# Performance work log

Measured on AMD Instinct MI355X. Metric: run time of the kernel, lower is better.

## Reference

```python
import jax, jax.numpy as jnp
import numpy as np

N, E = 50000, 600000
IN_DIM, HID, OUT_DIM = 128, 256, 64


def _sage_conv(x, edge_index, W_l, W_r, b):
    # PyG SAGEConv (mean aggr, root_weight=True):
    # out = mean_{j in N(i)} x_j @ W_l + x_i @ W_r + b
    src, dst = edge_index[0], edge_index[1]
    msg = x[src]  # [E, d] gather
    agg = jax.ops.segment_sum(msg, dst, num_segments=N)  # [N, d]
    cnt = jax.ops.segment_sum(jnp.ones((E,), dtype=x.dtype), dst, num_segments=N)
    agg = agg / jnp.maximum(cnt, 1.0)[:, None]
    return agg @ W_l + x @ W_r + b


def setup_inputs() -> dict:
    key = jax.random.key(0)
    ks = jax.random.split(key, 8)
    x = jax.random.normal(ks[0], (N, IN_DIM), dtype=jnp.float32)
    edge_index = jax.random.randint(ks[1], (2, E), 0, N, dtype=jnp.int64)
    s1 = 1.0 / np.sqrt(IN_DIM)
    s2 = 1.0 / np.sqrt(HID)
    W1_l = jax.random.uniform(ks[2], (IN_DIM, HID), jnp.float32, -s1, s1)
    W1_r = jax.random.uniform(ks[3], (IN_DIM, HID), jnp.float32, -s1, s1)
    b1 = jnp.zeros((HID,), jnp.float32)
    W2_l = jax.random.uniform(ks[4], (HID, OUT_DIM), jnp.float32, -s2, s2)
    W2_r = jax.random.uniform(ks[5], (HID, OUT_DIM), jnp.float32, -s2, s2)
    b2 = jnp.zeros((OUT_DIM,), jnp.float32)
    return {"x": x, "edge_index": edge_index, "W1_l": W1_l, "W1_r": W1_r,
            "b1": b1, "W2_l": W2_l, "W2_r": W2_r, "b2": b2}


def reference(x, edge_index, W1_l, W1_r, b1, W2_l, W2_r, b2):
    # SAGE.forward, eval mode (dropout = identity)
    h = jax.nn.relu(_sage_conv(x, edge_index, W1_l, W1_r, b1))
    out = _sage_conv(h, edge_index, W2_l, W2_r, b2)
    return out
```

## Files before the change

### kernel.cpp

```cpp
#include <hip/hip_runtime.h>

#define N_NODES 50000
#define N_EDGES 600000
#define N_PAD   50048
#define IN_DIM 128
#define HID 256
#define OUT_DIM 64
#define MAX_DEG 64
#define NBINS 196
#define BCAP 4096
#define NPART 256
#define ECHUNK 2344

typedef __attribute__((ext_vector_type(4))) float f32x4;
typedef __attribute__((ext_vector_type(8))) short short8;
typedef unsigned short u16;
typedef unsigned int u32;

__device__ __forceinline__ float bf2f(u32 lo16) {
  u32 u = lo16 << 16;
  return __builtin_bit_cast(float, u);
}
__device__ __forceinline__ u16 f2bf(float f) {
  u32 u = __builtin_bit_cast(u32, f);
  u = (u + 0x7FFF + ((u >> 16) & 1)) >> 16;
  return (u16)u;
}

#define SEG0 (N_PAD * 16)
#define SEG1 (SEG0 + 128 * 64)
#define SEG2 (SEG1 + 64 * 64)
#define PREP_TOT SEG2

__global__ void k_prep_part(const float* __restrict__ x,
                            const float* __restrict__ W1l, const float* __restrict__ W1r,
                            const float* __restrict__ W2l, const float* __restrict__ W2r,
                            const int* __restrict__ src, const int* __restrict__ dst,
                            u16* __restrict__ xb, u16* __restrict__ W1p,
                            u16* __restrict__ W2p, u32* __restrict__ region,
                            int* __restrict__ gcur) {
  if (blockIdx.x < NPART) {
    __shared__ int hist[256];
    __shared__ int base[256];
    const int t = threadIdx.x;
    hist[t] = 0;
    __syncthreads();
    const int e0 = blockIdx.x * ECHUNK;
    const int e1 = min(e0 + ECHUNK, N_EDGES);
    for (int e = e0 + t; e < e1; e += 256) atomicAdd(&hist[dst[e] >> 8], 1);
    __syncthreads();
    base[t] = (hist[t] > 0) ? atomicAdd(&gcur[t], hist[t]) : 0;
    hist[t] = 0;
    __syncthreads();
    for (int e = e0 + t; e < e1; e += 256) {
      int d = dst[e];
      int bin = d >> 8;
      int idx = base[bin] + atomicAdd(&hist[bin], 1);
      if (idx < BCAP)
        region[(size_t)bin * BCAP + idx] = (u32)(src[e] & 0xffff) | ((u32)(d & 255) << 16);
    }
    return;
  }
  int idx = (blockIdx.x - NPART) * 256 + threadIdx.x;
  if (idx < SEG0) {
    int row = idx >> 4;
    int c8 = (idx & 15) * 8;
    short8 o;
    if (row < N_NODES) {
      f32x4 a = *(const f32x4*)&x[(size_t)row * 128 + c8];
      f32x4 b = *(const f32x4*)&x[(size_t)row * 128 + c8 + 4];
      o[0] = (short)f2bf(a[0]); o[1] = (short)f2bf(a[1]);
      o[2] = (short)f2bf(a[2]); o[3] = (short)f2bf(a[3]);
      o[4] = (short)f2bf(b[0]); o[5] = (short)f2bf(b[1]);
      o[6] = (short)f2bf(b[2]); o[7] = (short)f2bf(b[3]);
    } else {
      for (int j = 0; j < 8; ++j) o[j] = 0;
    }
    *(short8*)&xb[(size_t)row * 128 + c8] = o;
  } else if (idx < SEG1) {
    int i = idx - SEG0;
    int F = i >> 6, l = i & 63;
    int wch = F >> 6, kt = (F >> 4) & 3, kk = (F >> 3) & 1, n = F & 7;
    int row = wch * 128 + n * 16 + (l & 15);
    int kb = kt * 64 + kk * 32 + (l >> 4) * 8;
    short8 o;
#pragma unroll
    for (int j = 0; j < 8; ++j) {
      int k = kb + j;
      float v = (k < 128) ? W1l[(size_t)k * HID + row] : W1r[(size_t)(k - 128) * HID + row];
      o[j] = (short)f2bf(v);
    }
    *(short8*)&W1p[(size_t)i * 8] = o;
  } else if (idx < SEG2) {
    int i = idx - SEG1;
    int G = i >> 6, l = i & 63;
    int wch = G >> 5, kk = (G >> 2) & 7, n = G & 3;
    int row = wch * 64 + n * 16 + (l & 15);
    int kb = kk * 32 + (l >> 4) * 8;
    short8 o;
#pragma unroll
    for (int j = 0; j < 8; ++j) {
      int k = kb + j;
      float v = (row < 64) ? W2l[(size_t)k * OUT_DIM + row]
                           : W2r[(size_t)k * OUT_DIM + (row - 64)];
      o[j] = (short)f2bf(v);
    }
    *(short8*)&W2p[(size_t)i * 8] = o;
  }
}


__global__ __launch_bounds__(256) void k_build(const u32* __restrict__ region,
                                               const int* __restrict__ gcur,
                                               int* __restrict__ cnt,
                                               u16* __restrict__ bucket) {
  __shared__ u16 lbkt[256 * 64];
  __shared__ int lcnt[256];
  const int t = threadIdx.x;
  const int bin = blockIdx.x;
  lcnt[t] = 0;
  __syncthreads();
  int n = gcur[bin];
  if (n > BCAP) n = BCAP;
  for (int i = t; i < n; i += 256) {
    u32 r = region[(size_t)bin * BCAP + i];
    int dl = (r >> 16) & 255;
    int pos = atomicAdd(&lcnt[dl], 1);
    if (pos < MAX_DEG) lbkt[dl * 64 + pos] = (u16)(r & 0xffff);
  }
  __syncthreads();
  int gnode = bin * 256 + t;
  if (gnode < N_NODES) cnt[gnode] = lcnt[t];
  for (int i = t; i < 2048; i += 256) {
    int nl = i >> 3, sub = i & 7;
    int gn = bin * 256 + nl;
    if (gn < N_NODES)
      *(short8*)&bucket[(size_t)gn * 64 + sub * 8] = *(const short8*)&lbkt[nl * 64 + sub * 8];
  }
}


__global__ void k_agg(const u16* __restrict__ xb, const int* __restrict__ cnt,
                      const u16* __restrict__ bucket, u16* __restrict__ agg) {
  int node = blockIdx.x * 4 + (threadIdx.x >> 6);
  if (node >= N_PAD) return;
  int lane = threadIdx.x & 63;
  int es = lane >> 4, dl = lane & 15;
  int deg = (node < N_NODES) ? cnt[node] : 0;
  int sreg = (node < N_NODES) ? (int)bucket[(size_t)node * MAX_DEG + lane] : 0;
  float acc[8] = {0.f, 0.f, 0.f, 0.f, 0.f, 0.f, 0.f, 0.f};
  short8 pend = (short8){0, 0, 0, 0, 0, 0, 0, 0};
  for (int e = 0; e < deg; e += 4) {
    int ee = e + es;
    int s = __shfl(sreg, ee & 63);
    short8 v = (short8){0, 0, 0, 0, 0, 0, 0, 0};
    if (ee < deg) v = *(const short8*)&xb[(size_t)s * 128 + dl * 8];
#pragma unroll
    for (int j = 0; j < 8; ++j) acc[j] += bf2f((u16)pend[j]);
    pend = v;
  }
#pragma unroll
  for (int j = 0; j < 8; ++j) acc[j] += bf2f((u16)pend[j]);
#pragma unroll
  for (int j = 0; j < 8; ++j) {
    acc[j] += __shfl_xor(acc[j], 16);
    acc[j] += __shfl_xor(acc[j], 32);
  }
  float inv = 1.f / fmaxf((float)deg, 1.f);
  if (es == 0) {
    short8 o;
#pragma unroll
    for (int j = 0; j < 8; ++j) o[j] = (short)f2bf(acc[j] * inv);
    *(short8*)&agg[(size_t)node * 128 + dl * 8] = o;
  }
}


__device__ __forceinline__ void gl_lds16(const void* g, void* l) {
  __builtin_amdgcn_global_load_lds((const __attribute__((address_space(1))) u32*)g,
                                   (__attribute__((address_space(3))) u32*)l, 16, 0, 0);
}

__global__ __launch_bounds__(256, 3) void k_mlp(
    const u16* __restrict__ agg, const u16* __restrict__ xb,
    const u16* __restrict__ W1p, const u16* __restrict__ W2p,
    const float* __restrict__ b1, u16* __restrict__ pb, u16* __restrict__ qb) {
  __shared__ u16 hs[64 * 256];
  __shared__ u16 As[2][64 * 64];
  const int t = threadIdx.x;
  const int wave = t >> 6;
  const int lane = t & 63;
  const int brow = blockIdx.x * 64;
  const int lr = lane & 15;
  const int kg = lane >> 4;
  const int wch = wave & 1;

  const int wr = (wave >> 1) * 32;
  const int wc = wch * 128;

  f32x4 acc[2][8];
#pragma unroll
  for (int m = 0; m < 2; ++m)
#pragma unroll
    for (int n = 0; n < 8; ++n) acc[m][n] = (f32x4){0.f, 0.f, 0.f, 0.f};

  auto stageA = [&](int buf, int kt) {
    const u16* base = (kt < 2) ? agg : xb;
    const int koff = (kt & 1) * 64;
#pragma unroll
    for (int i = 0; i < 2; ++i) {
      int chunk = wave * 2 + i;
      int f = chunk * 1024 + lane * 16;
      int row = f >> 7;
      int cbs = (f & 127) ^ ((row & 7) << 4);
      gl_lds16(&base[(size_t)(brow + row) * 128 + koff + (cbs >> 1)],
               (char*)As[buf] + chunk * 1024);
    }
  };

  stageA(0, 0);
  __syncthreads();

#pragma unroll
  for (int kt = 0; kt < 4; ++kt) {
    const int cur = kt & 1;
    if (kt < 3) stageA(cur ^ 1, kt + 1);
#pragma unroll
    for (int kk = 0; kk < 2; ++kk) {
      short8 af[2], bfr[8];
      const int cb = kk * 64 + kg * 16;
#pragma unroll
      for (int m = 0; m < 2; ++m) {
        int row = wr + m * 16 + lr;
        af[m] = *(const short8*)((const char*)As[cur] + row * 128 + (cb ^ ((row & 7) << 4)));
      }
#pragma unroll
      for (int n = 0; n < 8; ++n)
        bfr[n] = *(const short8*)&W1p[(size_t)(((wch * 4 + kt) * 2 + kk) * 8 + n) * 512 +
                                      lane * 8];
#pragma unroll
      for (int m = 0; m < 2; ++m)
#pragma unroll
        for (int n = 0; n < 8; ++n)
          acc[m][n] =
              __builtin_amdgcn_mfma_f32_16x16x32_bf16(af[m], bfr[n], acc[m][n], 0, 0, 0);
    }
    __syncthreads();
  }

#pragma unroll
  for (int n = 0; n < 8; ++n) {
    int col = wc + n * 16 + lr;
    float bv = b1[col];
#pragma unroll
    for (int m = 0; m < 2; ++m) {
#pragma unroll
      for (int j = 0; j < 4; ++j) {
        int row = wr + kg * 4 + m * 16 + j;
        float v = fmaxf(acc[m][n][j] + bv, 0.f);
        *(u16*)((char*)hs + row * 512 + ((col * 2) ^ ((row & 7) << 4))) = f2bf(v);
      }
    }
  }
  __syncthreads();

  const int wr2 = (wave >> 1) * 32;
  f32x4 acc2[2][4];
#pragma unroll
  for (int m = 0; m < 2; ++m)
#pragma unroll
    for (int n = 0; n < 4; ++n) acc2[m][n] = (f32x4){0.f, 0.f, 0.f, 0.f};

#pragma unroll
  for (int kk = 0; kk < 8; ++kk) {
    const int cb = kk * 64 + kg * 16;
    short8 af[2], bfr[4];
#pragma unroll
    for (int m = 0; m < 2; ++m) {
      int row = wr2 + m * 16 + lr;
      af[m] = *(const short8*)((const char*)hs + row * 512 + (cb ^ ((row & 7) << 4)));
    }
#pragma unroll
    for (int n = 0; n < 4; ++n)
      bfr[n] = *(const short8*)&W2p[(size_t)((wch * 8 + kk) * 4 + n) * 512 + lane * 8];
#pragma unroll
    for (int m = 0; m < 2; ++m)
#pragma unroll
      for (int n = 0; n < 4; ++n)
        acc2[m][n] =
            __builtin_amdgcn_mfma_f32_16x16x32_bf16(af[m], bfr[n], acc2[m][n], 0, 0, 0);
  }

  u16* outb = wch ? qb : pb;
#pragma unroll
  for (int n = 0; n < 4; ++n) {
    int col = n * 16 + lr;
#pragma unroll
    for (int m = 0; m < 2; ++m) {
#pragma unroll
      for (int j = 0; j < 4; ++j) {
        int row = brow + wr2 + kg * 4 + m * 16 + j;
        outb[(size_t)row * 64 + col] = f2bf(acc2[m][n][j]);
      }
    }
  }
}


__global__ void k_out(const u16* __restrict__ pb, const u16* __restrict__ qb,
                      const int* __restrict__ cnt, const u16* __restrict__ bucket,
                      const float* __restrict__ b2, float* __restrict__ out) {
  int node = blockIdx.x * 4 + (threadIdx.x >> 6);
  if (node >= N_NODES) return;
  int lane = threadIdx.x & 63;
  int es = lane >> 3, dl = lane & 7;
  int deg = cnt[node];
  int sreg = (int)bucket[(size_t)node * MAX_DEG + lane];
  float acc[8] = {0.f, 0.f, 0.f, 0.f, 0.f, 0.f, 0.f, 0.f};
  short8 pend = (short8){0, 0, 0, 0, 0, 0, 0, 0};
  for (int e = 0; e < deg; e += 8) {
    int ee = e + es;
    int s = __shfl(sreg, ee & 63);
    short8 v = (short8){0, 0, 0, 0, 0, 0, 0, 0};
    if (ee < deg) v = *(const short8*)&pb[(size_t)s * 64 + dl * 8];
#pragma unroll
    for (int j = 0; j < 8; ++j) acc[j] += bf2f((u16)pend[j]);
    pend = v;
  }
#pragma unroll
  for (int j = 0; j < 8; ++j) acc[j] += bf2f((u16)pend[j]);
#pragma unroll
  for (int j = 0; j < 8; ++j) {
    acc[j] += __shfl_xor(acc[j], 8);
    acc[j] += __shfl_xor(acc[j], 16);
    acc[j] += __shfl_xor(acc[j], 32);
  }
  float inv = 1.f / fmaxf((float)deg, 1.f);
  if (es == 0) {
    short8 q = *(const short8*)&qb[(size_t)node * 64 + dl * 8];
    f32x4 bb0 = *(const f32x4*)&b2[dl * 8];
    f32x4 bb1 = *(const f32x4*)&b2[dl * 8 + 4];
    f32x4 o0, o1;
#pragma unroll
    for (int j = 0; j < 4; ++j) {
      o0[j] = acc[j] * inv + bf2f((u16)q[j]) + bb0[j];
      o1[j] = acc[j + 4] * inv + bf2f((u16)q[j + 4]) + bb1[j];
    }
    *(f32x4*)&out[(size_t)node * 64 + dl * 8] = o0;
    *(f32x4*)&out[(size_t)node * 64 + dl * 8 + 4] = o1;
  }
}


extern "C" void kernel_launch(void* const* d_in, const int* in_sizes, int n_in,
                              void* d_out, int out_size, void* d_ws, size_t ws_size,
                              hipStream_t stream) {
  const float* x   = (const float*)d_in[0];
  const int*   ei  = (const int*)d_in[1];
  const float* W1l = (const float*)d_in[2];
  const float* W1r = (const float*)d_in[3];
  const float* b1  = (const float*)d_in[4];
  const float* W2l = (const float*)d_in[5];
  const float* W2r = (const float*)d_in[6];
  const float* b2  = (const float*)d_in[7];
  float* out = (float*)d_out;

  const int* src = ei;
  const int* dst = ei + N_EDGES;

  char* ws = (char*)d_ws;
  size_t off = 0;
  auto alloc = [&](size_t bytes) -> void* {
    void* p = ws + off;
    off = (off + bytes + 255) & ~(size_t)255;
    return p;
  };
  int* gcur   = (int*)alloc(256 * 4);
  u32* region = (u32*)alloc((size_t)NBINS * BCAP * 4);
  int* cnt    = (int*)alloc((size_t)N_NODES * 4);
  u16* bucket = (u16*)alloc((size_t)N_NODES * MAX_DEG * 2);
  u16* xb     = (u16*)alloc((size_t)N_PAD * 128 * 2);
  u16* agg    = (u16*)alloc((size_t)N_PAD * 128 * 2);
  u16* W1p    = (u16*)alloc((size_t)128 * 64 * 8 * 2);
  u16* W2p    = (u16*)alloc((size_t)64 * 64 * 8 * 2);
  u16* pb     = (u16*)alloc((size_t)N_PAD * 64 * 2);
  u16* qb     = (u16*)alloc((size_t)N_PAD * 64 * 2);

  hipMemsetAsync(gcur, 0, 256 * 4, stream);

  int blocks = NPART + (PREP_TOT + 255) / 256;
  k_prep_part<<<blocks, 256, 0, stream>>>(x, W1l, W1r, W2l, W2r, src, dst,
                                          xb, W1p, W2p, region, gcur);
  k_build<<<NBINS, 256, 0, stream>>>(region, gcur, cnt, bucket);
  k_agg<<<N_PAD / 4, 256, 0, stream>>>(xb, cnt, bucket, agg);
  k_mlp<<<N_PAD / 64, 256, 0, stream>>>(agg, xb, W1p, W2p, b1, pb, qb);
  k_out<<<(N_NODES + 3) / 4, 256, 0, stream>>>(pb, qb, cnt, bucket, b2, out);
}
```

Baseline: 102.2 us.

## Fuse neighbor mean aggregation into the layer-1 MLP kernel via shared memory

Removes the separate aggregation kernel and its global agg buffer. Each MLP block now gathers and averages its 64 nodes' neighbor features directly into swizzled LDS, while the self-feature tiles are prefetched into LDS at the same time. This saves a launch and the write and re-read of the aggregated activations. In exchange, each wave handles 16 nodes serially, so there is less parallelism for the latency-bound gather, and the LDS pressure may limit occupancy.

```diff
diff --git a/kernel.cpp b/kernel.cpp
--- a/kernel.cpp
+++ b/kernel.cpp
@@ -140,52 +140,17 @@
 }
 
 
-__global__ void k_agg(const u16* __restrict__ xb, const int* __restrict__ cnt,
-                      const u16* __restrict__ bucket, u16* __restrict__ agg) {
-  int node = blockIdx.x * 4 + (threadIdx.x >> 6);
-  if (node >= N_PAD) return;
-  int lane = threadIdx.x & 63;
-  int es = lane >> 4, dl = lane & 15;
-  int deg = (node < N_NODES) ? cnt[node] : 0;
-  int sreg = (node < N_NODES) ? (int)bucket[(size_t)node * MAX_DEG + lane] : 0;
-  float acc[8] = {0.f, 0.f, 0.f, 0.f, 0.f, 0.f, 0.f, 0.f};
-  short8 pend = (short8){0, 0, 0, 0, 0, 0, 0, 0};
-  for (int e = 0; e < deg; e += 4) {
-    int ee = e + es;
-    int s = __shfl(sreg, ee & 63);
-    short8 v = (short8){0, 0, 0, 0, 0, 0, 0, 0};
-    if (ee < deg) v = *(const short8*)&xb[(size_t)s * 128 + dl * 8];
-#pragma unroll
-    for (int j = 0; j < 8; ++j) acc[j] += bf2f((u16)pend[j]);
-    pend = v;
-  }
-#pragma unroll
-  for (int j = 0; j < 8; ++j) acc[j] += bf2f((u16)pend[j]);
-#pragma unroll
-  for (int j = 0; j < 8; ++j) {
-    acc[j] += __shfl_xor(acc[j], 16);
-    acc[j] += __shfl_xor(acc[j], 32);
-  }
-  float inv = 1.f / fmaxf((float)deg, 1.f);
-  if (es == 0) {
-    short8 o;
-#pragma unroll
-    for (int j = 0; j < 8; ++j) o[j] = (short)f2bf(acc[j] * inv);
-    *(short8*)&agg[(size_t)node * 128 + dl * 8] = o;
-  }
-}
-
-
 __device__ __forceinline__ void gl_lds16(const void* g, void* l) {
   __builtin_amdgcn_global_load_lds((const __attribute__((address_space(1))) u32*)g,
                                    (__attribute__((address_space(3))) u32*)l, 16, 0, 0);
 }
 
-__global__ __launch_bounds__(256, 3) void k_mlp(
-    const u16* __restrict__ agg, const u16* __restrict__ xb,
+__global__ __launch_bounds__(256, 3) void k_agg_mlp(
+    const u16* __restrict__ xb, const int* __restrict__ cnt,
+    const u16* __restrict__ bucket,
     const u16* __restrict__ W1p, const u16* __restrict__ W2p,
     const float* __restrict__ b1, u16* __restrict__ pb, u16* __restrict__ qb) {
-  __shared__ u16 hs[64 * 256];
+  __shared__ u16 un[64 * 256];
   __shared__ u16 As[2][64 * 64];
   const int t = threadIdx.x;
   const int wave = t >> 6;
@@ -195,36 +160,69 @@
   const int kg = lane >> 4;
   const int wch = wave & 1;
 
-  const int wr = (wave >> 1) * 32;
-  const int wc = wch * 128;
-
-  f32x4 acc[2][8];
-#pragma unroll
-  for (int m = 0; m < 2; ++m)
-#pragma unroll
-    for (int n = 0; n < 8; ++n) acc[m][n] = (f32x4){0.f, 0.f, 0.f, 0.f};
-
-  auto stageA = [&](int buf, int kt) {
-    const u16* base = (kt < 2) ? agg : xb;
-    const int koff = (kt & 1) * 64;
+#pragma unroll
+  for (int b = 0; b < 2; ++b) {
+    const int koff = b * 64;
 #pragma unroll
     for (int i = 0; i < 2; ++i) {
       int chunk = wave * 2 + i;
       int f = chunk * 1024 + lane * 16;
       int row = f >> 7;
       int cbs = (f & 127) ^ ((row & 7) << 4);
-      gl_lds16(&base[(size_t)(brow + row) * 128 + koff + (cbs >> 1)],
-               (char*)As[buf] + chunk * 1024);
-    }
-  };
-
-  stageA(0, 0);
-  __syncthreads();
+      gl_lds16(&xb[(size_t)(brow + row) * 128 + koff + (cbs >> 1)],
+               (char*)As[b] + chunk * 1024);
+    }
+  }
+
+  {
+    const int es = lane >> 4, dl = lane & 15;
+    for (int nl = 0; nl < 16; ++nl) {
+      int rowloc = wave * 16 + nl;
+      int node = brow + rowloc;
+      int deg = (node < N_NODES) ? cnt[node] : 0;
+      int sreg = (node < N_NODES) ? (int)bucket[(size_t)node * MAX_DEG + lane] : 0;
+      float acc[8] = {0.f, 0.f, 0.f, 0.f, 0.f, 0.f, 0.f, 0.f};
+      short8 pend = (short8){0, 0, 0, 0, 0, 0, 0, 0};
+      for (int e = 0; e < deg; e += 4) {
+        int ee = e + es;
+        int s = __shfl(sreg, ee & 63);
+        short8 v = (short8){0, 0, 0, 0, 0, 0, 0, 0};
+        if (ee < deg) v = *(const short8*)&xb[(size_t)s * 128 + dl * 8];
+#pragma unroll
+        for (int j = 0; j < 8; ++j) acc[j] += bf2f((u16)pend[j]);
+        pend = v;
+      }
+#pragma unroll
+      for (int j = 0; j < 8; ++j) acc[j] += bf2f((u16)pend[j]);
+#pragma unroll
+      for (int j = 0; j < 8; ++j) {
+        acc[j] += __shfl_xor(acc[j], 16);
+        acc[j] += __shfl_xor(acc[j], 32);
+      }
+      float inv = 1.f / fmaxf((float)deg, 1.f);
+      if (es == 0) {
+        short8 o;
+#pragma unroll
+        for (int j = 0; j < 8; ++j) o[j] = (short)f2bf(acc[j] * inv);
+        int b = dl >> 3, colb = (dl & 7) * 16;
+        *(short8*)((char*)un + b * 8192 + rowloc * 128 + (colb ^ ((rowloc & 7) << 4))) = o;
+      }
+    }
+  }
+  __syncthreads();
+
+  const int wr = (wave >> 1) * 32;
+  const int wc = wch * 128;
+
+  f32x4 acc1[2][8];
+#pragma unroll
+  for (int m = 0; m < 2; ++m)
+#pragma unroll
+    for (int n = 0; n < 8; ++n) acc1[m][n] = (f32x4){0.f, 0.f, 0.f, 0.f};
 
 #pragma unroll
   for (int kt = 0; kt < 4; ++kt) {
-    const int cur = kt & 1;
-    if (kt < 3) stageA(cur ^ 1, kt + 1);
+    const char* asrc = (kt < 2) ? ((const char*)un + kt * 8192) : (const char*)As[kt - 2];
 #pragma unroll
     for (int kk = 0; kk < 2; ++kk) {
       short8 af[2], bfr[8];
@@ -232,7 +230,7 @@
 #pragma unroll
       for (int m = 0; m < 2; ++m) {
         int row = wr + m * 16 + lr;
-        af[m] = *(const short8*)((const char*)As[cur] + row * 128 + (cb ^ ((row & 7) << 4)));
+        af[m] = *(const short8*)(asrc + row * 128 + (cb ^ ((row & 7) << 4)));
       }
 #pragma unroll
       for (int n = 0; n < 8; ++n)
@@ -242,11 +240,11 @@
       for (int m = 0; m < 2; ++m)
 #pragma unroll
         for (int n = 0; n < 8; ++n)
-          acc[m][n] =
-              __builtin_amdgcn_mfma_f32_16x16x32_bf16(af[m], bfr[n], acc[m][n], 0, 0, 0);
-    }
-    __syncthreads();
-  }
+          acc1[m][n] =
+              __builtin_amdgcn_mfma_f32_16x16x32_bf16(af[m], bfr[n], acc1[m][n], 0, 0, 0);
+    }
+  }
+  __syncthreads();
 
 #pragma unroll
   for (int n = 0; n < 8; ++n) {
@@ -257,8 +255,8 @@
 #pragma unroll
       for (int j = 0; j < 4; ++j) {
         int row = wr + kg * 4 + m * 16 + j;
-        float v = fmaxf(acc[m][n][j] + bv, 0.f);
-        *(u16*)((char*)hs + row * 512 + ((col * 2) ^ ((row & 7) << 4))) = f2bf(v);
+        float v = fmaxf(acc1[m][n][j] + bv, 0.f);
+        *(u16*)((char*)un + row * 512 + ((col * 2) ^ ((row & 7) << 4))) = f2bf(v);
       }
     }
   }
@@ -278,7 +276,7 @@
 #pragma unroll
     for (int m = 0; m < 2; ++m) {
       int row = wr2 + m * 16 + lr;
-      af[m] = *(const short8*)((const char*)hs + row * 512 + (cb ^ ((row & 7) << 4)));
+      af[m] = *(const short8*)((const char*)un + row * 512 + (cb ^ ((row & 7) << 4)));
     }
 #pragma unroll
     for (int n = 0; n < 4; ++n)
@@ -380,7 +378,6 @@
   int* cnt    = (int*)alloc((size_t)N_NODES * 4);
   u16* bucket = (u16*)alloc((size_t)N_NODES * MAX_DEG * 2);
   u16* xb     = (u16*)alloc((size_t)N_PAD * 128 * 2);
-  u16* agg    = (u16*)alloc((size_t)N_PAD * 128 * 2);
   u16* W1p    = (u16*)alloc((size_t)128 * 64 * 8 * 2);
   u16* W2p    = (u16*)alloc((size_t)64 * 64 * 8 * 2);
   u16* pb     = (u16*)alloc((size_t)N_PAD * 64 * 2);
@@ -392,7 +389,6 @@
   k_prep_part<<<blocks, 256, 0, stream>>>(x, W1l, W1r, W2l, W2r, src, dst,
                                           xb, W1p, W2p, region, gcur);
   k_build<<<NBINS, 256, 0, stream>>>(region, gcur, cnt, bucket);
-  k_agg<<<N_PAD / 4, 256, 0, stream>>>(xb, cnt, bucket, agg);
-  k_mlp<<<N_PAD / 64, 256, 0, stream>>>(agg, xb, W1p, W2p, b1, pb, qb);
+  k_agg_mlp<<<N_PAD / 64, 256, 0, stream>>>(xb, cnt, bucket, W1p, W2p, b1, pb, qb);
   k_out<<<(N_NODES + 3) / 4, 256, 0, stream>>>(pb, qb, cnt, bucket, b2, out);
 }
```

Result: slower. 135.9 us (+32.9%).
